# Performance work log

Hardware: AMD Instinct MI355X
Metric: run time of the kernel (lower is better)

## Reference

```python
import jax, jax.numpy as jnp
import numpy as np

B, HW, N, C, F, ITERS = 32, 4096, 16, 128, 512, 3
EPS_LN = 1e-5
EPS_ATTN = 1e-5


def _ln(x, g, b):
    m = x.mean(-1, keepdims=True)
    v = ((x - m) ** 2).mean(-1, keepdims=True)
    return (x - m) / jnp.sqrt(v + EPS_LN) * g + b


def _gru(x, h, wih, whh, bih, bhh):
    # torch.nn.GRUCell math
    gi = x @ wih.T + bih
    gh = h @ whh.T + bhh
    i_r, i_z, i_n = jnp.split(gi, 3, axis=-1)
    h_r, h_z, h_n = jnp.split(gh, 3, axis=-1)
    r = jax.nn.sigmoid(i_r + h_r)
    z = jax.nn.sigmoid(i_z + h_z)
    n = jnp.tanh(i_n + r * h_n)
    return (1.0 - z) * n + z * h


def setup_inputs() -> dict:
    key = jax.random.key(0)
    ks = jax.random.split(key, 16)
    s = 0.02
    d = {
        'inp': jax.random.normal(ks[0], (B, HW, C), jnp.float32),
        'query': jax.random.normal(ks[1], (B, N, C), jnp.float32),
        'ln_kv_g': jnp.ones((C,), jnp.float32),
        'ln_kv_b': jnp.zeros((C,), jnp.float32),
        'Wk': jax.random.normal(ks[2], (C, C), jnp.float32) * s,
        'Wv': jax.random.normal(ks[3], (C, C), jnp.float32) * s,
        'ln_q_g': jnp.ones((C,), jnp.float32),
        'ln_q_b': jnp.zeros((C,), jnp.float32),
        'Wq': jax.random.normal(ks[4], (C, C), jnp.float32) * s,
        'gru_wih': jax.random.normal(ks[5], (3 * C, C), jnp.float32) * s,
        'gru_whh': jax.random.normal(ks[6], (3 * C, C), jnp.float32) * s,
        'gru_bih': jnp.zeros((3 * C,), jnp.float32),
        'gru_bhh': jnp.zeros((3 * C,), jnp.float32),
        'ln2_g': jnp.ones((C,), jnp.float32),
        'ln2_b': jnp.zeros((C,), jnp.float32),
        'ffn_w1': jax.random.normal(ks[7], (F, C), jnp.float32) * s,
        'ffn_b1': jnp.zeros((F,), jnp.float32),
        'ffn_w2': jax.random.normal(ks[8], (C, F), jnp.float32) * s,
        'ffn_b2': jnp.zeros((C,), jnp.float32),
    }
    return d


def reference(inp, query, ln_kv_g, ln_kv_b, Wk, Wv, ln_q_g, ln_q_b, Wq,
              gru_wih, gru_whh, gru_bih, gru_bhh, ln2_g, ln2_b,
              ffn_w1, ffn_b1, ffn_w2, ffn_b2):
    b, n, c = query.shape
    kv = _ln(inp, ln_kv_g, ln_kv_b)
    k = kv @ Wk.T  # (b, hw, c)
    v = kv @ Wv.T  # (b, hw, c)
    scale = c ** -0.5
    q = query
    a0 = None
    for _ in range(ITERS):
        x = q
        qn = _ln(q, ln_q_g, ln_q_b) @ Wq.T
        logit = jnp.einsum('bqc,bkc->bqk', qn * scale, k)  # (b, n, hw)
        a0 = jax.nn.softmax(logit, axis=1)  # inverted: softmax over slots
        a = a0 / (a0.sum(2, keepdims=True) + EPS_ATTN)  # renorm over keys
        u = jnp.einsum('bqk,bkc->bqc', a, v)
        y = _gru(u.reshape(b * n, c), x.reshape(b * n, c),
                 gru_wih, gru_whh, gru_bih, gru_bhh).reshape(b, n, c)
        z = _ln(y, ln2_g, ln2_b)
        ffn = jax.nn.relu(z @ ffn_w1.T + ffn_b1) @ ffn_w2.T + ffn_b2
        q = y + ffn
    return (q, a0)
```

## Files before the change

kernel.cpp:

```cpp
#include <hip/hip_runtime.h>
#include <math.h>

#define B_ 32
#define HW_ 4096
#define N_ 16
#define C_ 128
#define F_ 512
#define ITERS_ 3
#define EPS_LN 1e-5f
#define EPS_ATTN 1e-5f

typedef __attribute__((ext_vector_type(8))) short short8;
typedef __attribute__((ext_vector_type(4))) float f32x4;

static __device__ __forceinline__ unsigned short f2b(float f) {
    union { float f; unsigned u; } v; v.f = f;
    unsigned r = v.u + 0x7fffu + ((v.u >> 16) & 1u);
    return (unsigned short)(r >> 16);
}
static __device__ __forceinline__ float blo(unsigned u) {
    union { unsigned u; float f; } v; v.u = u << 16; return v.f;
}
static __device__ __forceinline__ float bhi(unsigned u) {
    union { unsigned u; float f; } v; v.u = u & 0xffff0000u; return v.f;
}
static __device__ __forceinline__ void gload_lds16(const void* g, void* l) {
    __builtin_amdgcn_global_load_lds(
        (const __attribute__((address_space(1))) unsigned int*)g,
        (__attribute__((address_space(3))) unsigned int*)l, 16, 0, 0);
}

__global__ __launch_bounds__(256) void k_prep(
    const float* __restrict__ Wk, const float* __restrict__ Wv,
    const float* __restrict__ wih, const float* __restrict__ whh,
    const float* __restrict__ w1, const float* __restrict__ w2,
    unsigned short* __restrict__ Wk_sw, unsigned short* __restrict__ Wv_sw,
    unsigned short* __restrict__ wihT, unsigned short* __restrict__ whhT,
    unsigned short* __restrict__ w1T, unsigned short* __restrict__ w2T,
    const float* __restrict__ query, const float* __restrict__ lnqg,
    const float* __restrict__ lnqb, const float* __restrict__ Wq,
    float* __restrict__ wqTf, unsigned short* __restrict__ qn_g)
{
    __shared__ __align__(16) float xq[16 * 128];
    int tid = threadIdx.x;
    int blk = blockIdx.x;
    if (blk < 32) {
        int t = blk * 256 + tid;
        const float* src; unsigned short* dst; int off;
        if (t < 4096) { src = Wk; dst = Wk_sw; off = t; }
        else          { src = Wv; dst = Wv_sw; off = t - 4096; }
        float4 a = ((const float4*)src)[off];
        uint2 p;
        p.x = (unsigned)f2b(a.x) | ((unsigned)f2b(a.y) << 16);
        p.y = (unsigned)f2b(a.z) | ((unsigned)f2b(a.w) << 16);
        int r = off >> 5;
        int j = off & 31;
        int cg = j >> 1, half = j & 1;
        int dsw = r * 128 + (((cg ^ (r & 7)) << 3)) + (half << 2);
        *(uint2*)(dst + dsw) = p;
        return;
    }
    if (blk < 256) {
        const float* src; unsigned short* dst; int o, g, id, Cin;
        if (blk < 80) {
            id = (blk - 32) * 256 + tid;
            g = id / 384; o = id - g * 384;
            src = wih; dst = wihT; Cin = 128;
        } else if (blk < 128) {
            id = (blk - 80) * 256 + tid;
            g = id / 384; o = id - g * 384;
            src = whh; dst = whhT; Cin = 128;
        } else if (blk < 192) {
            id = (blk - 128) * 256 + tid;
            g = id >> 9; o = id & 511;
            src = w1; dst = w1T; Cin = 128;
        } else {
            id = (blk - 192) * 256 + tid;
            g = id >> 7; o = id & 127;
            src = w2; dst = w2T; Cin = 512;
        }
        float4 a = *(const float4*)(src + o * Cin + g * 4);
        uint2 p;
        p.x = (unsigned)f2b(a.x) | ((unsigned)f2b(a.y) << 16);
        p.y = (unsigned)f2b(a.z) | ((unsigned)f2b(a.w) << 16);
        *(uint2*)(dst + id * 4) = p;
        return;
    }
    if (blk >= 288) {
        int t = (blk - 288) * 256 + tid;
        int c = t & 127, g = t >> 7;
        float4 a = *(const float4*)(Wq + c * 128 + g * 4);
        ((float4*)wqTf)[g * 128 + c] = a;
        return;
    }
    int b = blk - 256;
    int n = tid >> 4, part = tid & 15;
    int row = b * 16 + n;
    const float4* x4 = (const float4*)(query + row * 128 + part * 8);
    float4 x0 = x4[0], x1 = x4[1];
    float s = x0.x + x0.y + x0.z + x0.w + x1.x + x1.y + x1.z + x1.w;
    float ss = x0.x * x0.x + x0.y * x0.y + x0.z * x0.z + x0.w * x0.w +
               x1.x * x1.x + x1.y * x1.y + x1.z * x1.z + x1.w * x1.w;
    s += __shfl_xor(s, 1); s += __shfl_xor(s, 2); s += __shfl_xor(s, 4); s += __shfl_xor(s, 8);
    ss += __shfl_xor(ss, 1); ss += __shfl_xor(ss, 2); ss += __shfl_xor(ss, 4); ss += __shfl_xor(ss, 8);
    float mean = s * (1.f / 128.f);
    float var = ss * (1.f / 128.f) - mean * mean;
    float rstd = rsqrtf(var + EPS_LN);
    const float4* g4 = (const float4*)(lnqg + part * 8);
    const float4* b4 = (const float4*)(lnqb + part * 8);
    float4 g0 = g4[0], g1 = g4[1], bb0 = b4[0], bb1 = b4[1];
    float4 o0, o1;
    o0.x = (x0.x - mean) * rstd * g0.x + bb0.x;
    o0.y = (x0.y - mean) * rstd * g0.y + bb0.y;
    o0.z = (x0.z - mean) * rstd * g0.z + bb0.z;
    o0.w = (x0.w - mean) * rstd * g0.w + bb0.w;
    o1.x = (x1.x - mean) * rstd * g1.x + bb1.x;
    o1.y = (x1.y - mean) * rstd * g1.y + bb1.y;
    o1.z = (x1.z - mean) * rstd * g1.z + bb1.z;
    o1.w = (x1.w - mean) * rstd * g1.w + bb1.w;
    float4* xrow = (float4*)&xq[n * 128];
    xrow[part * 2] = o0;
    xrow[part * 2 + 1] = o1;
    __syncthreads();
    float o[8] = {0.f, 0.f, 0.f, 0.f, 0.f, 0.f, 0.f, 0.f};
    const float4* xv4 = (const float4*)&xq[n * 128];
#pragma unroll 4
    for (int j = 0; j < 32; j++) {
        float4 xv = xv4[j];
#pragma unroll
        for (int i = 0; i < 8; i++) {
            float4 w = ((const float4*)(Wq + (part * 8 + i) * 128))[j];
            o[i] += w.x * xv.x + w.y * xv.y + w.z * xv.z + w.w * xv.w;
        }
    }
    const float scale = 0.08838834764831845f;
#pragma unroll
    for (int i = 0; i < 8; i++)
        qn_g[row * 128 + part * 8 + i] = f2b(o[i] * scale);
}

__global__ __launch_bounds__(512, 4) void k_kvproj(
    const float* __restrict__ inp, const float* __restrict__ lng,
    const float* __restrict__ lnb, const unsigned short* __restrict__ Wk_sw,
    const unsigned short* __restrict__ Wv_sw, unsigned short* __restrict__ Kbf,
    unsigned short* __restrict__ Vt)
{
    __shared__ __align__(16) unsigned short W_lds[128 * 128];
    __shared__ __align__(16) unsigned short T_lds[128 * 132];
    const int tid = threadIdx.x;
    const int wave = tid >> 6, lane = tid & 63;
    const int l15 = lane & 15, q4 = lane >> 4;
    const int kof = q4 * 8;
    const int tile0 = blockIdx.x * 128;
    const int b = tile0 >> 12;
    const int hwbase = tile0 & (HW_ - 1);

    {
        const char* gw = (const char*)Wk_sw + wave * 4096 + lane * 16;
        char* lw = (char*)W_lds + wave * 4096;
#pragma unroll
        for (int j = 0; j < 4; j++)
            gload_lds16(gw + j * 1024, lw + j * 1024);
    }

    float x[4][8];
    {
        const float* rowp = inp + (tile0 + (wave << 4) + l15) * C_;
        float s = 0.f, ss = 0.f;
#pragma unroll
        for (int ks = 0; ks < 4; ks++) {
#pragma unroll
            for (int h = 0; h < 2; h++) {
                float4 v = *(const float4*)(rowp + ks * 32 + kof + h * 4);
                x[ks][h * 4 + 0] = v.x; x[ks][h * 4 + 1] = v.y;
                x[ks][h * 4 + 2] = v.z; x[ks][h * 4 + 3] = v.w;
                s += v.x + v.y + v.z + v.w;
                ss += v.x * v.x + v.y * v.y + v.z * v.z + v.w * v.w;
            }
        }
        s += __shfl_xor(s, 16);  s += __shfl_xor(s, 32);
        ss += __shfl_xor(ss, 16); ss += __shfl_xor(ss, 32);
        float mean = s * (1.f / 128.f);
        float var = ss * (1.f / 128.f) - mean * mean;
        float rstd = rsqrtf(var + EPS_LN);
#pragma unroll
        for (int ks = 0; ks < 4; ks++) {
#pragma unroll
            for (int h = 0; h < 2; h++) {
                float4 g = *(const float4*)(lng + ks * 32 + kof + h * 4);
                float4 bb = *(const float4*)(lnb + ks * 32 + kof + h * 4);
                x[ks][h * 4 + 0] = (x[ks][h * 4 + 0] - mean) * rstd * g.x + bb.x;
                x[ks][h * 4 + 1] = (x[ks][h * 4 + 1] - mean) * rstd * g.y + bb.y;
                x[ks][h * 4 + 2] = (x[ks][h * 4 + 2] - mean) * rstd * g.z + bb.z;
                x[ks][h * 4 + 3] = (x[ks][h * 4 + 3] - mean) * rstd * g.w + bb.w;
            }
        }
    }
    short8 af[4];
#pragma unroll
    for (int ks = 0; ks < 4; ks++) {
        union { short8 s8; unsigned u[4]; } p;
#pragma unroll
        for (int j = 0; j < 4; j++)
            p.u[j] = (unsigned)f2b(x[ks][2 * j]) | ((unsigned)f2b(x[ks][2 * j + 1]) << 16);
        af[ks] = p.s8;
    }

    __syncthreads();

    f32x4 acc[8];
#pragma unroll
    for (int nt = 0; nt < 8; nt++) {
        acc[nt] = (f32x4){0.f, 0.f, 0.f, 0.f};
#pragma unroll
        for (int ks = 0; ks < 4; ks++) {
            short8 bf = *(const short8*)&W_lds[(nt * 16 + l15) * 128 + ((ks * 4 + q4) ^ (l15 & 7)) * 8];
            acc[nt] = __builtin_amdgcn_mfma_f32_16x16x32_bf16(af[ks], bf, acc[nt], 0, 0, 0);
        }
    }
#pragma unroll
    for (int nt = 0; nt < 8; nt++) {
        int c = nt * 16 + l15;
#pragma unroll
        for (int i = 0; i < 4; i++)
            T_lds[((wave << 4) + (q4 << 2) + i) * 132 + c] = f2b(acc[nt][i]);
    }
    __syncthreads();

    {
        int row = tid >> 2, part = tid & 3;
        uint4* dst = (uint4*)&Kbf[(b * HW_ + hwbase + row) * C_ + part * 32];
#pragma unroll
        for (int j = 0; j < 4; j++)
            dst[j] = *(const uint4*)&T_lds[row * 132 + part * 32 + j * 8];
    }
    {
        const char* gw = (const char*)Wv_sw + wave * 4096 + lane * 16;
        char* lw = (char*)W_lds + wave * 4096;
#pragma unroll
        for (int j = 0; j < 4; j++)
            gload_lds16(gw + j * 1024, lw + j * 1024);
    }
    __syncthreads();

#pragma unroll
    for (int nt = 0; nt < 8; nt++) {
        acc[nt] = (f32x4){0.f, 0.f, 0.f, 0.f};
#pragma unroll
        for (int ks = 0; ks < 4; ks++) {
            short8 bf = *(const short8*)&W_lds[(nt * 16 + l15) * 128 + ((ks * 4 + q4) ^ (l15 & 7)) * 8];
            acc[nt] = __builtin_amdgcn_mfma_f32_16x16x32_bf16(af[ks], bf, acc[nt], 0, 0, 0);
        }
    }
#pragma unroll
    for (int nt = 0; nt < 8; nt++) {
        int c = nt * 16 + l15;
#pragma unroll
        for (int i = 0; i < 4; i++)
            T_lds[c * 132 + (wave << 4) + (q4 << 2) + i] = f2b(acc[nt][i]);
    }
    __syncthreads();

    {
        int c = tid >> 2, part = tid & 3;
        uint4* dst = (uint4*)&Vt[(b * C_ + c) * HW_ + hwbase + part * 32];
#pragma unroll
        for (int j = 0; j < 4; j++)
            dst[j] = *(const uint4*)&T_lds[c * 132 + part * 32 + j * 8];
    }
}

__global__ __launch_bounds__(256) void k_attn(
    const unsigned short* __restrict__ qn_g, const unsigned short* __restrict__ Kbf,
    const unsigned short* __restrict__ Vt, float* __restrict__ Upart,
    float* __restrict__ rspart, float* __restrict__ a0_out, int last)
{
    __shared__ __align__(16) unsigned short Pb[4][16 * 40];
    __shared__ float rsw[4][16];
    const int b = blockIdx.y, chunk = blockIdx.x;
    const int tid = threadIdx.x;
    const int wave = tid >> 6, lane = tid & 63;
    const int l15 = lane & 15, q4 = lane >> 4;
    const int kof = q4 * 8;
    const int hwb = chunk * 128 + wave * 32;
    const int cbase = wave * 32;

    short8 aq[4];
#pragma unroll
    for (int ks = 0; ks < 4; ks++)
        aq[ks] = *(const short8*)&qn_g[(b * 16 + l15) * 128 + ks * 32 + kof];
    short8 av[2][4];
#pragma unroll
    for (int ct = 0; ct < 2; ct++) {
#pragma unroll
        for (int kc = 0; kc < 4; kc++)
            av[ct][kc] = *(const short8*)&Vt[(b * C_ + cbase + ct * 16 + l15) * HW_
                                             + chunk * 128 + kc * 32 + kof];
    }

    unsigned short* Pw = &Pb[wave][0];
    float rs[4] = {0.f, 0.f, 0.f, 0.f};
#pragma unroll
    for (int s = 0; s < 2; s++) {
        int hwt = hwb + s * 16;
        f32x4 sa = {0.f, 0.f, 0.f, 0.f};
#pragma unroll
        for (int ks = 0; ks < 4; ks++) {
            short8 bk = *(const short8*)&Kbf[(b * HW_ + hwt + l15) * C_ + ks * 32 + kof];
            sa = __builtin_amdgcn_mfma_f32_16x16x32_bf16(aq[ks], bk, sa, 0, 0, 0);
        }
        float mx = fmaxf(fmaxf(sa[0], sa[1]), fmaxf(sa[2], sa[3]));
        mx = fmaxf(mx, __shfl_xor(mx, 16));
        mx = fmaxf(mx, __shfl_xor(mx, 32));
        float e[4]; float ssum = 0.f;
#pragma unroll
        for (int i = 0; i < 4; i++) { e[i] = __expf(sa[i] - mx); ssum += e[i]; }
        ssum += __shfl_xor(ssum, 16);
        ssum += __shfl_xor(ssum, 32);
        float inv = 1.f / ssum;
#pragma unroll
        for (int i = 0; i < 4; i++) {
            float a0v = e[i] * inv;
            rs[i] += a0v;
            if (last) a0_out[(b * 16 + q4 * 4 + i) * HW_ + hwt + l15] = a0v;
            Pw[(q4 * 4 + i) * 40 + s * 16 + l15] = f2b(a0v);
        }
    }
#pragma unroll
    for (int i = 0; i < 4; i++) {
        rs[i] += __shfl_xor(rs[i], 1);
        rs[i] += __shfl_xor(rs[i], 2);
        rs[i] += __shfl_xor(rs[i], 4);
        rs[i] += __shfl_xor(rs[i], 8);
    }
    if (l15 == 0) {
#pragma unroll
        for (int i = 0; i < 4; i++) rsw[wave][q4 * 4 + i] = rs[i];
    }
    __syncthreads();

    f32x4 ua0 = {0.f, 0.f, 0.f, 0.f}, ua1 = {0.f, 0.f, 0.f, 0.f};
#pragma unroll
    for (int kc = 0; kc < 4; kc++) {
        short8 bp = *(const short8*)&Pb[kc][l15 * 40 + kof];
        ua0 = __builtin_amdgcn_mfma_f32_16x16x32_bf16(av[0][kc], bp, ua0, 0, 0, 0);
        ua1 = __builtin_amdgcn_mfma_f32_16x16x32_bf16(av[1][kc], bp, ua1, 0, 0, 0);
    }
    {
        float* up = Upart + (b * 32 + chunk) * 2048;
        *(f32x4*)&up[l15 * 128 + cbase + (q4 << 2)] = ua0;
        *(f32x4*)&up[l15 * 128 + cbase + 16 + (q4 << 2)] = ua1;
        if (tid < 16)
            rspart[(b * 32 + chunk) * 16 + tid] =
                rsw[0][tid] + rsw[1][tid] + rsw[2][tid] + rsw[3][tid];
    }
}

__global__ __launch_bounds__(512) void k_tail(
    const float* __restrict__ Upart, const float* __restrict__ rspart,
    const float* __restrict__ hsrc, float* __restrict__ q_buf,
    const unsigned short* __restrict__ wihT, const unsigned short* __restrict__ whhT,
    const float* __restrict__ bih, const float* __restrict__ bhh,
    const float* __restrict__ ln2g, const float* __restrict__ ln2b,
    const unsigned short* __restrict__ w1T, const float* __restrict__ b1,
    const unsigned short* __restrict__ w2T, const float* __restrict__ b2,
    const float* __restrict__ lnqg, const float* __restrict__ lnqb,
    const float* __restrict__ wqTf, unsigned short* __restrict__ qn_g,
    float* __restrict__ out_q, int last)
{
    __shared__ __align__(16) float red0[512], red1[512];
    __shared__ __align__(16) float u0_l[128], u1_l[128];
    __shared__ __align__(16) float h0_l[128], h1_l[128];
    __shared__ __align__(16) float y0_l[128], y1_l[128];
    __shared__ __align__(16) float z0_l[128], z1_l[128];
    __shared__ __align__(16) float g0_l[768], g1_l[768];
    __shared__ __align__(16) float f0_l[512], f1_l[512];
    __shared__ float srs0, srs1;
    const int tid = threadIdx.x;
    const int row0 = blockIdx.x * 2, row1 = row0 + 1;
    const int b = row0 >> 4, q0 = row0 & 15;

    {
        int c = tid & 127, h = tid >> 7;
        const float* upA = Upart + (b * 32 + h * 8) * 2048 + q0 * 128 + c;
        float a = 0.f, bv = 0.f;
#pragma unroll
        for (int ch = 0; ch < 8; ch++) {
            a  += upA[ch * 2048];
            bv += upA[ch * 2048 + 128];
        }
        red0[tid] = a; red1[tid] = bv;
        if (tid < 128) h0_l[tid] = hsrc[row0 * 128 + tid];
        else if (tid < 256) h1_l[tid - 128] = hsrc[row1 * 128 + (tid - 128)];
        if (tid >= 256 && tid < 288) {
            int t = tid - 256;
            float v = rspart[(b * 32 + t) * 16 + q0];
            v += __shfl_xor(v, 1); v += __shfl_xor(v, 2); v += __shfl_xor(v, 4);
            v += __shfl_xor(v, 8); v += __shfl_xor(v, 16);
            if (t == 0) srs0 = v;
        }
        if (tid >= 320 && tid < 352) {
            int t = tid - 320;
            float v = rspart[(b * 32 + t) * 16 + q0 + 1];
            v += __shfl_xor(v, 1); v += __shfl_xor(v, 2); v += __shfl_xor(v, 4);
            v += __shfl_xor(v, 8); v += __shfl_xor(v, 16);
            if (t == 0) srs1 = v;
        }
    }
    __syncthreads();
    if (tid < 128) {
        float s = red0[tid] + red0[tid + 128] + red0[tid + 256] + red0[tid + 384];
        u0_l[tid] = s / (srs0 + EPS_ATTN);
    } else if (tid < 256) {
        int c = tid - 128;
        float s = red1[c] + red1[c + 128] + red1[c + 256] + red1[c + 384];
        u1_l[c] = s / (srs1 + EPS_ATTN);
    }
    __syncthreads();
    {
        int o = tid;
        const uint2* wp; const float *sA, *sB; float bias;
        if (o < 384) { wp = (const uint2*)wihT + o; sA = u0_l; sB = u1_l; bias = bih[o]; }
        else         { wp = (const uint2*)whhT + (o - 384); sA = h0_l; sB = h1_l; bias = bhh[o - 384]; }
        float fa = 0.f, fb = 0.f;
#pragma unroll 4
        for (int g = 0; g < 32; g++) {
            uint2 w = wp[g * 384];
            float4 a4 = *(const float4*)&sA[g * 4];
            float4 b4 = *(const float4*)&sB[g * 4];
            float w0 = blo(w.x), w1v = bhi(w.x), w2v = blo(w.y), w3 = bhi(w.y);
            fa += w0 * a4.x + w1v * a4.y + w2v * a4.z + w3 * a4.w;
            fb += w0 * b4.x + w1v * b4.y + w2v * b4.z + w3 * b4.w;
        }
        g0_l[o] = fa + bias; g1_l[o] = fb + bias;
        if (tid < 256) {
            int o2 = tid + 512;
            const uint2* wp2 = (const uint2*)whhT + (o2 - 384);
            float fa2 = 0.f, fb2 = 0.f;
#pragma unroll 4
            for (int g = 0; g < 32; g++) {
                uint2 w = wp2[g * 384];
                float4 a4 = *(const float4*)&h0_l[g * 4];
                float4 b4 = *(const float4*)&h1_l[g * 4];
                float w0 = blo(w.x), w1v = bhi(w.x), w2v = blo(w.y), w3 = bhi(w.y);
                fa2 += w0 * a4.x + w1v * a4.y + w2v * a4.z + w3 * a4.w;
                fb2 += w0 * b4.x + w1v * b4.y + w2v * b4.z + w3 * b4.w;
            }
            float bias2 = bhh[o2 - 384];
            g0_l[o2] = fa2 + bias2; g1_l[o2] = fb2 + bias2;
        }
    }
    __syncthreads();
    if (tid < 256) {
        int c = tid & 127, r = tid >> 7;
        const float* gl = r ? g1_l : g0_l;
        const float* hl = r ? h1_l : h0_l;
        float* yl = r ? y1_l : y0_l;
        float ir = gl[c], iz = gl[128 + c], in_ = gl[256 + c];
        float hr = gl[384 + c], hz = gl[512 + c], hn = gl[640 + c];
        float rr = 1.f / (1.f + expf(-(ir + hr)));
        float zz = 1.f / (1.f + expf(-(iz + hz)));
        float nn = tanhf(in_ + rr * hn);
        yl[c] = (1.f - zz) * nn + zz * hl[c];
    }
    __syncthreads();
    {
        int r = tid >> 8;
        const float* yl = r ? y1_l : y0_l;
        int l = tid & 63;
        float v0 = yl[l], v1 = yl[l + 64];
        float s = v0 + v1, ss = v0 * v0 + v1 * v1;
#pragma unroll
        for (int off = 1; off < 64; off <<= 1) {
            s += __shfl_xor(s, off);
            ss += __shfl_xor(ss, off);
        }
        float mean = s * (1.f / 128.f);
        float var = ss * (1.f / 128.f) - mean * mean;
        float rstd = rsqrtf(var + EPS_LN);
        int c = tid & 255;
        if (c < 128) {
            float* zl = r ? z1_l : z0_l;
            zl[c] = (yl[c] - mean) * rstd * ln2g[c] + ln2b[c];
        }
    }
    __syncthreads();
    {
        const uint2* wp = (const uint2*)w1T + tid;
        float fa = 0.f, fb = 0.f;
#pragma unroll 4
        for (int g = 0; g < 32; g++) {
            uint2 w = wp[g * 512];
            float4 za = *(const float4*)&z0_l[g * 4];
            float4 zb = *(const float4*)&z1_l[g * 4];
            float w0 = blo(w.x), w1v = bhi(w.x), w2v = blo(w.y), w3 = bhi(w.y);
            fa += w0 * za.x + w1v * za.y + w2v * za.z + w3 * za.w;
            fb += w0 * zb.x + w1v * zb.y + w2v * zb.z + w3 * zb.w;
        }
        float bb = b1[tid];
        f0_l[tid] = fmaxf(fa + bb, 0.f);
        f1_l[tid] = fmaxf(fb + bb, 0.f);
    }
    __syncthreads();
    {
        int c = tid & 127, k4 = tid >> 7;
        const uint2* wp = (const uint2*)w2T + c;
        float fa = 0.f, fb = 0.f;
#pragma unroll 4
        for (int j = 0; j < 32; j++) {
            int g = k4 * 32 + j;
            uint2 w = wp[g * 128];
            float4 ha = *(const float4*)&f0_l[g * 4];
            float4 hb = *(const float4*)&f1_l[g * 4];
            float w0 = blo(w.x), w1v = bhi(w.x), w2v = blo(w.y), w3 = bhi(w.y);
            fa += w0 * ha.x + w1v * ha.y + w2v * ha.z + w3 * ha.w;
            fb += w0 * hb.x + w1v * hb.y + w2v * hb.z + w3 * hb.w;
        }
        red0[tid] = fa; red1[tid] = fb;
    }
    __syncthreads();
    if (tid < 128) {
        float f2 = red0[tid] + red0[tid + 128] + red0[tid + 256] + red0[tid + 384];
        float qn = y0_l[tid] + f2 + b2[tid];
        u0_l[tid] = qn;
        q_buf[row0 * 128 + tid] = qn;
        if (last) out_q[row0 * 128 + tid] = qn;
    } else if (tid < 256) {
        int c = tid - 128;
        float f2 = red1[c] + red1[c + 128] + red1[c + 256] + red1[c + 384];
        float qn = y1_l[c] + f2 + b2[c];
        u1_l[c] = qn;
        q_buf[row1 * 128 + c] = qn;
        if (last) out_q[row1 * 128 + c] = qn;
    }
    if (last) return;
    __syncthreads();
    {
        int r = tid >> 8;
        const float* yl = r ? u1_l : u0_l;
        int l = tid & 63;
        float v0 = yl[l], v1 = yl[l + 64];
        float s = v0 + v1, ss = v0 * v0 + v1 * v1;
#pragma unroll
        for (int off = 1; off < 64; off <<= 1) {
            s += __shfl_xor(s, off);
            ss += __shfl_xor(ss, off);
        }
        float mean = s * (1.f / 128.f);
        float var = ss * (1.f / 128.f) - mean * mean;
        float rstd = rsqrtf(var + EPS_LN);
        int c = tid & 255;
        if (c < 128) {
            float* zl = r ? z1_l : z0_l;
            zl[c] = (yl[c] - mean) * rstd * lnqg[c] + lnqb[c];
        }
    }
    __syncthreads();
    {
        int c = tid & 127, k4 = tid >> 7;
        const float4* wp = (const float4*)wqTf + c;
        float fa = 0.f, fb = 0.f;
#pragma unroll
        for (int j = 0; j < 8; j++) {
            int g = k4 * 8 + j;
            float4 w = wp[g * 128];
            float4 za = *(const float4*)&z0_l[g * 4];
            float4 zb = *(const float4*)&z1_l[g * 4];
            fa += w.x * za.x + w.y * za.y + w.z * za.z + w.w * za.w;
            fb += w.x * zb.x + w.y * zb.y + w.z * zb.z + w.w * zb.w;
        }
        red0[tid] = fa; red1[tid] = fb;
    }
    __syncthreads();
    if (tid < 128) {
        float qa = red0[tid] + red0[tid + 128] + red0[tid + 256] + red0[tid + 384];
        qn_g[row0 * 128 + tid] = f2b(qa * 0.08838834764831845f);
    } else if (tid < 256) {
        int c = tid - 128;
        float qa = red1[c] + red1[c + 128] + red1[c + 256] + red1[c + 384];
        qn_g[row1 * 128 + c] = f2b(qa * 0.08838834764831845f);
    }
}

extern "C" void kernel_launch(void* const* d_in, const int* in_sizes, int n_in,
                              void* d_out, int out_size, void* d_ws, size_t ws_size,
                              hipStream_t stream) {
    const float* inp     = (const float*)d_in[0];
    const float* query   = (const float*)d_in[1];
    const float* ln_kv_g = (const float*)d_in[2];
    const float* ln_kv_b = (const float*)d_in[3];
    const float* Wk      = (const float*)d_in[4];
    const float* Wv      = (const float*)d_in[5];
    const float* ln_q_g  = (const float*)d_in[6];
    const float* ln_q_b  = (const float*)d_in[7];
    const float* Wq      = (const float*)d_in[8];
    const float* gru_wih = (const float*)d_in[9];
    const float* gru_whh = (const float*)d_in[10];
    const float* gru_bih = (const float*)d_in[11];
    const float* gru_bhh = (const float*)d_in[12];
    const float* ln2_g   = (const float*)d_in[13];
    const float* ln2_b   = (const float*)d_in[14];
    const float* ffn_w1  = (const float*)d_in[15];
    const float* ffn_b1  = (const float*)d_in[16];
    const float* ffn_w2  = (const float*)d_in[17];
    const float* ffn_b2  = (const float*)d_in[18];

    char* ws = (char*)d_ws;
    unsigned short* Kbf    = (unsigned short*)ws;
    unsigned short* Vt     = (unsigned short*)(ws + 33554432);
    float* q_buf           = (float*)(ws + 67108864);
    float* Upart           = (float*)(ws + 67371008);
    float* rspart          = (float*)(ws + 75759616);
    unsigned short* qn_g   = (unsigned short*)(ws + 75825152);
    unsigned short* Wk_sw  = (unsigned short*)(ws + 75956224);
    unsigned short* Wv_sw  = (unsigned short*)(ws + 75988992);
    unsigned short* wihT   = (unsigned short*)(ws + 76021760);
    unsigned short* whhT   = (unsigned short*)(ws + 76120064);
    unsigned short* w1T    = (unsigned short*)(ws + 76218368);
    unsigned short* w2T    = (unsigned short*)(ws + 76349440);
    float* wqTf            = (float*)(ws + 76480512);

    float* out_q  = (float*)d_out;
    float* out_a0 = out_q + B_ * N_ * C_;

    k_prep<<<dim3(304), dim3(256), 0, stream>>>(
        Wk, Wv, gru_wih, gru_whh, ffn_w1, ffn_w2,
        Wk_sw, Wv_sw, wihT, whhT, w1T, w2T,
        query, ln_q_g, ln_q_b, Wq, wqTf, qn_g);
    k_kvproj<<<dim3((B_ * HW_) / 128), dim3(512), 0, stream>>>(
        inp, ln_kv_g, ln_kv_b, Wk_sw, Wv_sw, Kbf, Vt);

    for (int it = 0; it < ITERS_; it++) {
        int last = (it == ITERS_ - 1) ? 1 : 0;
        const float* hsrc = (it == 0) ? query : q_buf;
        k_attn<<<dim3(32, B_), dim3(256), 0, stream>>>(
            qn_g, Kbf, Vt, Upart, rspart, out_a0, last);
        k_tail<<<dim3((B_ * N_) / 2), dim3(512), 0, stream>>>(
            Upart, rspart, hsrc, q_buf, wihT, whhT, gru_bih, gru_bhh,
            ln2_g, ln2_b, w1T, ffn_b1, w2T, ffn_b2,
            ln_q_g, ln_q_b, wqTf, qn_g, out_q, last);
    }
}
```

Measured before the change: 281.2 us.

## Fuse attention and tail iterations into one persistent kernel with per-batch flags

Replaces the six per-iteration k_attn/k_tail launches with a single persistent 256-block kernel. Each group of 8 blocks handles one batch and coordinates through global atomic flags with acquire/release ordering instead of kernel boundaries. This removes launch overhead and lets batches progress independently. In exchange, correctness depends on all 256 blocks being co-resident, there is spin-wait cost, and each block now handles four attention chunks in sequence.

Result: slower. 614.0 us (+118.3%).

```diff
diff --git a/kernel.cpp b/kernel.cpp
--- a/kernel.cpp
+++ b/kernel.cpp
@@ -28,6 +28,19 @@
     __builtin_amdgcn_global_load_lds(
         (const __attribute__((address_space(1))) unsigned int*)g,
         (__attribute__((address_space(3))) unsigned int*)l, 16, 0, 0);
+}
+static __device__ __forceinline__ void postflag(unsigned* f) {
+    __threadfence();
+    __syncthreads();
+    if (threadIdx.x == 0)
+        __hip_atomic_fetch_add(f, 1u, __ATOMIC_RELEASE, __HIP_MEMORY_SCOPE_AGENT);
+}
+static __device__ __forceinline__ void waitflag(unsigned* f, unsigned target) {
+    if (threadIdx.x == 0) {
+        while (__hip_atomic_load(f, __ATOMIC_ACQUIRE, __HIP_MEMORY_SCOPE_AGENT) < target)
+            __builtin_amdgcn_s_sleep(2);
+    }
+    __syncthreads();
 }
 
 __global__ __launch_bounds__(256) void k_prep(
@@ -55,8 +68,8 @@
         p.y = (unsigned)f2b(a.z) | ((unsigned)f2b(a.w) << 16);
         int r = off >> 5;
         int j = off & 31;
-        int cg = j >> 1, half = j & 1;
-        int dsw = r * 128 + (((cg ^ (r & 7)) << 3)) + (half << 2);
+        int cg2 = j >> 1, half = j & 1;
+        int dsw = r * 128 + (((cg2 ^ (r & 7)) << 3)) + (half << 2);
         *(uint2*)(dst + dsw) = p;
         return;
     }
@@ -270,104 +283,22 @@
     }
 }
 
-__global__ __launch_bounds__(256) void k_attn(
-    const unsigned short* __restrict__ qn_g, const unsigned short* __restrict__ Kbf,
-    const unsigned short* __restrict__ Vt, float* __restrict__ Upart,
-    float* __restrict__ rspart, float* __restrict__ a0_out, int last)
-{
-    __shared__ __align__(16) unsigned short Pb[4][16 * 40];
-    __shared__ float rsw[4][16];
-    const int b = blockIdx.y, chunk = blockIdx.x;
-    const int tid = threadIdx.x;
-    const int wave = tid >> 6, lane = tid & 63;
-    const int l15 = lane & 15, q4 = lane >> 4;
-    const int kof = q4 * 8;
-    const int hwb = chunk * 128 + wave * 32;
-    const int cbase = wave * 32;
-
-    short8 aq[4];
-#pragma unroll
-    for (int ks = 0; ks < 4; ks++)
-        aq[ks] = *(const short8*)&qn_g[(b * 16 + l15) * 128 + ks * 32 + kof];
-    short8 av[2][4];
-#pragma unroll
-    for (int ct = 0; ct < 2; ct++) {
-#pragma unroll
-        for (int kc = 0; kc < 4; kc++)
-            av[ct][kc] = *(const short8*)&Vt[(b * C_ + cbase + ct * 16 + l15) * HW_
-                                             + chunk * 128 + kc * 32 + kof];
-    }
-
-    unsigned short* Pw = &Pb[wave][0];
-    float rs[4] = {0.f, 0.f, 0.f, 0.f};
-#pragma unroll
-    for (int s = 0; s < 2; s++) {
-        int hwt = hwb + s * 16;
-        f32x4 sa = {0.f, 0.f, 0.f, 0.f};
-#pragma unroll
-        for (int ks = 0; ks < 4; ks++) {
-            short8 bk = *(const short8*)&Kbf[(b * HW_ + hwt + l15) * C_ + ks * 32 + kof];
-            sa = __builtin_amdgcn_mfma_f32_16x16x32_bf16(aq[ks], bk, sa, 0, 0, 0);
-        }
-        float mx = fmaxf(fmaxf(sa[0], sa[1]), fmaxf(sa[2], sa[3]));
-        mx = fmaxf(mx, __shfl_xor(mx, 16));
-        mx = fmaxf(mx, __shfl_xor(mx, 32));
-        float e[4]; float ssum = 0.f;
-#pragma unroll
-        for (int i = 0; i < 4; i++) { e[i] = __expf(sa[i] - mx); ssum += e[i]; }
-        ssum += __shfl_xor(ssum, 16);
-        ssum += __shfl_xor(ssum, 32);
-        float inv = 1.f / ssum;
-#pragma unroll
-        for (int i = 0; i < 4; i++) {
-            float a0v = e[i] * inv;
-            rs[i] += a0v;
-            if (last) a0_out[(b * 16 + q4 * 4 + i) * HW_ + hwt + l15] = a0v;
-            Pw[(q4 * 4 + i) * 40 + s * 16 + l15] = f2b(a0v);
-        }
-    }
-#pragma unroll
-    for (int i = 0; i < 4; i++) {
-        rs[i] += __shfl_xor(rs[i], 1);
-        rs[i] += __shfl_xor(rs[i], 2);
-        rs[i] += __shfl_xor(rs[i], 4);
-        rs[i] += __shfl_xor(rs[i], 8);
-    }
-    if (l15 == 0) {
-#pragma unroll
-        for (int i = 0; i < 4; i++) rsw[wave][q4 * 4 + i] = rs[i];
-    }
-    __syncthreads();
-
-    f32x4 ua0 = {0.f, 0.f, 0.f, 0.f}, ua1 = {0.f, 0.f, 0.f, 0.f};
-#pragma unroll
-    for (int kc = 0; kc < 4; kc++) {
-        short8 bp = *(const short8*)&Pb[kc][l15 * 40 + kof];
-        ua0 = __builtin_amdgcn_mfma_f32_16x16x32_bf16(av[0][kc], bp, ua0, 0, 0, 0);
-        ua1 = __builtin_amdgcn_mfma_f32_16x16x32_bf16(av[1][kc], bp, ua1, 0, 0, 0);
-    }
-    {
-        float* up = Upart + (b * 32 + chunk) * 2048;
-        *(f32x4*)&up[l15 * 128 + cbase + (q4 << 2)] = ua0;
-        *(f32x4*)&up[l15 * 128 + cbase + 16 + (q4 << 2)] = ua1;
-        if (tid < 16)
-            rspart[(b * 32 + chunk) * 16 + tid] =
-                rsw[0][tid] + rsw[1][tid] + rsw[2][tid] + rsw[3][tid];
-    }
-}
-
-__global__ __launch_bounds__(512) void k_tail(
-    const float* __restrict__ Upart, const float* __restrict__ rspart,
-    const float* __restrict__ hsrc, float* __restrict__ q_buf,
+__global__ __launch_bounds__(512, 2) void k_fused(
+    const float* __restrict__ query, float* __restrict__ q_buf,
+    const unsigned short* __restrict__ Kbf, const unsigned short* __restrict__ Vt,
+    unsigned short* __restrict__ qn_g, float* __restrict__ Upart,
+    float* __restrict__ rspart, float* __restrict__ a0_out,
     const unsigned short* __restrict__ wihT, const unsigned short* __restrict__ whhT,
     const float* __restrict__ bih, const float* __restrict__ bhh,
     const float* __restrict__ ln2g, const float* __restrict__ ln2b,
     const unsigned short* __restrict__ w1T, const float* __restrict__ b1,
     const unsigned short* __restrict__ w2T, const float* __restrict__ b2,
     const float* __restrict__ lnqg, const float* __restrict__ lnqb,
-    const float* __restrict__ wqTf, unsigned short* __restrict__ qn_g,
-    float* __restrict__ out_q, int last)
+    const float* __restrict__ wqTf, float* __restrict__ out_q,
+    unsigned* __restrict__ flags)
 {
+    __shared__ __align__(16) unsigned short Pb[2][4][16 * 40];
+    __shared__ float rsw[2][4][16];
     __shared__ __align__(16) float red0[512], red1[512];
     __shared__ __align__(16) float u0_l[128], u1_l[128];
     __shared__ __align__(16) float h0_l[128], h1_l[128];
@@ -376,209 +307,310 @@
     __shared__ __align__(16) float g0_l[768], g1_l[768];
     __shared__ __align__(16) float f0_l[512], f1_l[512];
     __shared__ float srs0, srs1;
+
     const int tid = threadIdx.x;
-    const int row0 = blockIdx.x * 2, row1 = row0 + 1;
-    const int b = row0 >> 4, q0 = row0 & 15;
-
-    {
-        int c = tid & 127, h = tid >> 7;
-        const float* upA = Upart + (b * 32 + h * 8) * 2048 + q0 * 128 + c;
-        float a = 0.f, bv = 0.f;
-#pragma unroll
-        for (int ch = 0; ch < 8; ch++) {
-            a  += upA[ch * 2048];
-            bv += upA[ch * 2048 + 128];
-        }
-        red0[tid] = a; red1[tid] = bv;
-        if (tid < 128) h0_l[tid] = hsrc[row0 * 128 + tid];
-        else if (tid < 256) h1_l[tid - 128] = hsrc[row1 * 128 + (tid - 128)];
-        if (tid >= 256 && tid < 288) {
-            int t = tid - 256;
-            float v = rspart[(b * 32 + t) * 16 + q0];
-            v += __shfl_xor(v, 1); v += __shfl_xor(v, 2); v += __shfl_xor(v, 4);
-            v += __shfl_xor(v, 8); v += __shfl_xor(v, 16);
-            if (t == 0) srs0 = v;
-        }
-        if (tid >= 320 && tid < 352) {
-            int t = tid - 320;
-            float v = rspart[(b * 32 + t) * 16 + q0 + 1];
-            v += __shfl_xor(v, 1); v += __shfl_xor(v, 2); v += __shfl_xor(v, 4);
-            v += __shfl_xor(v, 8); v += __shfl_xor(v, 16);
-            if (t == 0) srs1 = v;
-        }
-    }
-    __syncthreads();
-    if (tid < 128) {
-        float s = red0[tid] + red0[tid + 128] + red0[tid + 256] + red0[tid + 384];
-        u0_l[tid] = s / (srs0 + EPS_ATTN);
-    } else if (tid < 256) {
-        int c = tid - 128;
-        float s = red1[c] + red1[c + 128] + red1[c + 256] + red1[c + 384];
-        u1_l[c] = s / (srs1 + EPS_ATTN);
-    }
-    __syncthreads();
-    {
-        int o = tid;
-        const uint2* wp; const float *sA, *sB; float bias;
-        if (o < 384) { wp = (const uint2*)wihT + o; sA = u0_l; sB = u1_l; bias = bih[o]; }
-        else         { wp = (const uint2*)whhT + (o - 384); sA = h0_l; sB = h1_l; bias = bhh[o - 384]; }
-        float fa = 0.f, fb = 0.f;
+    const int bid = blockIdx.x;
+    const int b = bid >> 3;
+    unsigned* flagA = flags;
+    unsigned* flagQ = flags + 96;
+
+    const int half = tid >> 8;
+    const int cw = (tid >> 6) & 3;
+    const int lane = tid & 63;
+    const int l15 = lane & 15, q4 = lane >> 4;
+    const int kof = q4 * 8;
+    const int cbase = cw * 32;
+
+    for (int it = 0; it < ITERS_; ++it) {
+        const int last = (it == ITERS_ - 1);
+        if (it > 0) waitflag(&flagQ[it * 32 + b], 8);
+
+        short8 aq[4];
+#pragma unroll
+        for (int ks = 0; ks < 4; ks++)
+            aq[ks] = *(const short8*)&qn_g[(b * 16 + l15) * 128 + ks * 32 + kof];
+        for (int r = 0; r < 2; ++r) {
+            const int chunk = (bid & 7) * 4 + r * 2 + half;
+            const int hwb = chunk * 128 + cw * 32;
+
+            short8 av[2][4];
+#pragma unroll
+            for (int ct = 0; ct < 2; ct++) {
+#pragma unroll
+                for (int kc = 0; kc < 4; kc++)
+                    av[ct][kc] = *(const short8*)&Vt[(b * C_ + cbase + ct * 16 + l15) * HW_
+                                                     + chunk * 128 + kc * 32 + kof];
+            }
+            unsigned short* Pw = &Pb[half][cw][0];
+            float rs[4] = {0.f, 0.f, 0.f, 0.f};
+#pragma unroll
+            for (int s = 0; s < 2; s++) {
+                int hwt = hwb + s * 16;
+                f32x4 sa = {0.f, 0.f, 0.f, 0.f};
+#pragma unroll
+                for (int ks = 0; ks < 4; ks++) {
+                    short8 bk = *(const short8*)&Kbf[(b * HW_ + hwt + l15) * C_ + ks * 32 + kof];
+                    sa = __builtin_amdgcn_mfma_f32_16x16x32_bf16(aq[ks], bk, sa, 0, 0, 0);
+                }
+                float mx = fmaxf(fmaxf(sa[0], sa[1]), fmaxf(sa[2], sa[3]));
+                mx = fmaxf(mx, __shfl_xor(mx, 16));
+                mx = fmaxf(mx, __shfl_xor(mx, 32));
+                float e[4]; float ssum = 0.f;
+#pragma unroll
+                for (int i = 0; i < 4; i++) { e[i] = __expf(sa[i] - mx); ssum += e[i]; }
+                ssum += __shfl_xor(ssum, 16);
+                ssum += __shfl_xor(ssum, 32);
+                float inv = 1.f / ssum;
+#pragma unroll
+                for (int i = 0; i < 4; i++) {
+                    float a0v = e[i] * inv;
+                    rs[i] += a0v;
+                    if (last) a0_out[(b * 16 + q4 * 4 + i) * HW_ + hwt + l15] = a0v;
+                    Pw[(q4 * 4 + i) * 40 + s * 16 + l15] = f2b(a0v);
+                }
+            }
+#pragma unroll
+            for (int i = 0; i < 4; i++) {
+                rs[i] += __shfl_xor(rs[i], 1);
+                rs[i] += __shfl_xor(rs[i], 2);
+                rs[i] += __shfl_xor(rs[i], 4);
+                rs[i] += __shfl_xor(rs[i], 8);
+            }
+            if (l15 == 0) {
+#pragma unroll
+                for (int i = 0; i < 4; i++) rsw[half][cw][q4 * 4 + i] = rs[i];
+            }
+            __syncthreads();
+
+            f32x4 ua0 = {0.f, 0.f, 0.f, 0.f}, ua1 = {0.f, 0.f, 0.f, 0.f};
+#pragma unroll
+            for (int kc = 0; kc < 4; kc++) {
+                short8 bp = *(const short8*)&Pb[half][kc][l15 * 40 + kof];
+                ua0 = __builtin_amdgcn_mfma_f32_16x16x32_bf16(av[0][kc], bp, ua0, 0, 0, 0);
+                ua1 = __builtin_amdgcn_mfma_f32_16x16x32_bf16(av[1][kc], bp, ua1, 0, 0, 0);
+            }
+            {
+                float* up = Upart + (b * 32 + chunk) * 2048;
+                *(f32x4*)&up[l15 * 128 + cbase + (q4 << 2)] = ua0;
+                *(f32x4*)&up[l15 * 128 + cbase + 16 + (q4 << 2)] = ua1;
+                if ((tid & 255) < 16) {
+                    int t = tid & 15;
+                    rspart[(b * 32 + chunk) * 16 + t] =
+                        rsw[half][0][t] + rsw[half][1][t] + rsw[half][2][t] + rsw[half][3][t];
+                }
+            }
+            __syncthreads();
+        }
+        postflag(&flagA[it * 32 + b]);
+        waitflag(&flagA[it * 32 + b], 8);
+
+        {
+            const int row0 = bid * 2, row1 = row0 + 1;
+            const int q0 = row0 & 15;
+            const float* hsrc = (it == 0) ? query : q_buf;
+            {
+                int c = tid & 127, h = tid >> 7;
+                const float* upA = Upart + (b * 32 + h * 8) * 2048 + q0 * 128 + c;
+                float a = 0.f, bv = 0.f;
+#pragma unroll
+                for (int ch = 0; ch < 8; ch++) {
+                    a  += upA[ch * 2048];
+                    bv += upA[ch * 2048 + 128];
+                }
+                red0[tid] = a; red1[tid] = bv;
+                if (tid < 128) h0_l[tid] = hsrc[row0 * 128 + tid];
+                else if (tid < 256) h1_l[tid - 128] = hsrc[row1 * 128 + (tid - 128)];
+                if (tid >= 256 && tid < 288) {
+                    int t = tid - 256;
+                    float v = rspart[(b * 32 + t) * 16 + q0];
+                    v += __shfl_xor(v, 1); v += __shfl_xor(v, 2); v += __shfl_xor(v, 4);
+                    v += __shfl_xor(v, 8); v += __shfl_xor(v, 16);
+                    if (t == 0) srs0 = v;
+                }
+                if (tid >= 320 && tid < 352) {
+                    int t = tid - 320;
+                    float v = rspart[(b * 32 + t) * 16 + q0 + 1];
+                    v += __shfl_xor(v, 1); v += __shfl_xor(v, 2); v += __shfl_xor(v, 4);
+                    v += __shfl_xor(v, 8); v += __shfl_xor(v, 16);
+                    if (t == 0) srs1 = v;
+                }
+            }
+            __syncthreads();
+            if (tid < 128) {
+                float s = red0[tid] + red0[tid + 128] + red0[tid + 256] + red0[tid + 384];
+                u0_l[tid] = s / (srs0 + EPS_ATTN);
+            } else if (tid < 256) {
+                int c = tid - 128;
+                float s = red1[c] + red1[c + 128] + red1[c + 256] + red1[c + 384];
+                u1_l[c] = s / (srs1 + EPS_ATTN);
+            }
+            __syncthreads();
+            {
+                int o = tid;
+                const uint2* wp; const float *sA, *sB; float bias;
+                if (o < 384) { wp = (const uint2*)wihT + o; sA = u0_l; sB = u1_l; bias = bih[o]; }
+                else         { wp = (const uint2*)whhT + (o - 384); sA = h0_l; sB = h1_l; bias = bhh[o - 384]; }
+                float fa = 0.f, fb = 0.f;
 #pragma unroll 4
-        for (int g = 0; g < 32; g++) {
-            uint2 w = wp[g * 384];
-            float4 a4 = *(const float4*)&sA[g * 4];
-            float4 b4 = *(const float4*)&sB[g * 4];
-            float w0 = blo(w.x), w1v = bhi(w.x), w2v = blo(w.y), w3 = bhi(w.y);
-            fa += w0 * a4.x + w1v * a4.y + w2v * a4.z + w3 * a4.w;
-            fb += w0 * b4.x + w1v * b4.y + w2v * b4.z + w3 * b4.w;
-        }
-        g0_l[o] = fa + bias; g1_l[o] = fb + bias;
-        if (tid < 256) {
-            int o2 = tid + 512;
-            const uint2* wp2 = (const uint2*)whhT + (o2 - 384);
-            float fa2 = 0.f, fb2 = 0.f;
+                for (int g = 0; g < 32; g++) {
+                    uint2 w = wp[g * 384];
+                    float4 a4 = *(const float4*)&sA[g * 4];
+                    float4 b4 = *(const float4*)&sB[g * 4];
+                    float w0 = blo(w.x), w1v = bhi(w.x), w2v = blo(w.y), w3 = bhi(w.y);
+                    fa += w0 * a4.x + w1v * a4.y + w2v * a4.z + w3 * a4.w;
+                    fb += w0 * b4.x + w1v * b4.y + w2v * b4.z + w3 * b4.w;
+                }
+                g0_l[o] = fa + bias; g1_l[o] = fb + bias;
+                if (tid < 256) {
+                    int o2 = tid + 512;
+                    const uint2* wp2 = (const uint2*)whhT + (o2 - 384);
+                    float fa2 = 0.f, fb2 = 0.f;
 #pragma unroll 4
-            for (int g = 0; g < 32; g++) {
-                uint2 w = wp2[g * 384];
-                float4 a4 = *(const float4*)&h0_l[g * 4];
-                float4 b4 = *(const float4*)&h1_l[g * 4];
-                float w0 = blo(w.x), w1v = bhi(w.x), w2v = blo(w.y), w3 = bhi(w.y);
-                fa2 += w0 * a4.x + w1v * a4.y + w2v * a4.z + w3 * a4.w;
-                fb2 += w0 * b4.x + w1v * b4.y + w2v * b4.z + w3 * b4.w;
-            }
-            float bias2 = bhh[o2 - 384];
-            g0_l[o2] = fa2 + bias2; g1_l[o2] = fb2 + bias2;
-        }
-    }
-    __syncthreads();
-    if (tid < 256) {
-        int c = tid & 127, r = tid >> 7;
-        const float* gl = r ? g1_l : g0_l;
-        const float* hl = r ? h1_l : h0_l;
-        float* yl = r ? y1_l : y0_l;
-        float ir = gl[c], iz = gl[128 + c], in_ = gl[256 + c];
-        float hr = gl[384 + c], hz = gl[512 + c], hn = gl[640 + c];
-        float rr = 1.f / (1.f + expf(-(ir + hr)));
-        float zz = 1.f / (1.f + expf(-(iz + hz)));
-        float nn = tanhf(in_ + rr * hn);
-        yl[c] = (1.f - zz) * nn + zz * hl[c];
-    }
-    __syncthreads();
-    {
-        int r = tid >> 8;
-        const float* yl = r ? y1_l : y0_l;
-        int l = tid & 63;
-        float v0 = yl[l], v1 = yl[l + 64];
-        float s = v0 + v1, ss = v0 * v0 + v1 * v1;
-#pragma unroll
-        for (int off = 1; off < 64; off <<= 1) {
-            s += __shfl_xor(s, off);
-            ss += __shfl_xor(ss, off);
-        }
-        float mean = s * (1.f / 128.f);
-        float var = ss * (1.f / 128.f) - mean * mean;
-        float rstd = rsqrtf(var + EPS_LN);
-        int c = tid & 255;
-        if (c < 128) {
-            float* zl = r ? z1_l : z0_l;
-            zl[c] = (yl[c] - mean) * rstd * ln2g[c] + ln2b[c];
-        }
-    }
-    __syncthreads();
-    {
-        const uint2* wp = (const uint2*)w1T + tid;
-        float fa = 0.f, fb = 0.f;
+                    for (int g = 0; g < 32; g++) {
+                        uint2 w = wp2[g * 384];
+                        float4 a4 = *(const float4*)&h0_l[g * 4];
+                        float4 b4 = *(const float4*)&h1_l[g * 4];
+                        float w0 = blo(w.x), w1v = bhi(w.x), w2v = blo(w.y), w3 = bhi(w.y);
+                        fa2 += w0 * a4.x + w1v * a4.y + w2v * a4.z + w3 * a4.w;
+                        fb2 += w0 * b4.x + w1v * b4.y + w2v * b4.z + w3 * b4.w;
+                    }
+                    float bias2 = bhh[o2 - 384];
+                    g0_l[o2] = fa2 + bias2; g1_l[o2] = fb2 + bias2;
+                }
+            }
+            __syncthreads();
+            if (tid < 256) {
+                int c = tid & 127, r = tid >> 7;
+                const float* gl = r ? g1_l : g0_l;
+                const float* hl = r ? h1_l : h0_l;
+                float* yl = r ? y1_l : y0_l;
+                float ir = gl[c], iz = gl[128 + c], in_ = gl[256 + c];
+                float hr = gl[384 + c], hz = gl[512 + c], hn = gl[640 + c];
+                float rr = 1.f / (1.f + expf(-(ir + hr)));
+                float zz = 1.f / (1.f + expf(-(iz + hz)));
+                float nn = tanhf(in_ + rr * hn);
+                yl[c] = (1.f - zz) * nn + zz * hl[c];
+            }
+            __syncthreads();
+            {
+                int r = tid >> 8;
+                const float* yl = r ? y1_l : y0_l;
+                int l = tid & 63;
+                float v0 = yl[l], v1 = yl[l + 64];
+                float s = v0 + v1, ss = v0 * v0 + v1 * v1;
+#pragma unroll
+                for (int off = 1; off < 64; off <<= 1) {
+                    s += __shfl_xor(s, off);
+                    ss += __shfl_xor(ss, off);
+                }
+                float mean = s * (1.f / 128.f);
+                float var = ss * (1.f / 128.f) - mean * mean;
+                float rstd = rsqrtf(var + EPS_LN);
+                int c = tid & 255;
+                if (c < 128) {
+                    float* zl = r ? z1_l : z0_l;
+                    zl[c] = (yl[c] - mean) * rstd * ln2g[c] + ln2b[c];
+                }
+            }
+            __syncthreads();
+            {
+                const uint2* wp = (const uint2*)w1T + tid;
+                float fa = 0.f, fb = 0.f;
 #pragma unroll 4
-        for (int g = 0; g < 32; g++) {
-            uint2 w = wp[g * 512];
-            float4 za = *(const float4*)&z0_l[g * 4];
-            float4 zb = *(const float4*)&z1_l[g * 4];
-            float w0 = blo(w.x), w1v = bhi(w.x), w2v = blo(w.y), w3 = bhi(w.y);
-            fa += w0 * za.x + w1v * za.y + w2v * za.z + w3 * za.w;
-            fb += w0 * zb.x + w1v * zb.y + w2v * zb.z + w3 * zb.w;
-        }
-        float bb = b1[tid];
-        f0_l[tid] = fmaxf(fa + bb, 0.f);
-        f1_l[tid] = fmaxf(fb + bb, 0.f);
-    }
-    __syncthreads();
-    {
-        int c = tid & 127, k4 = tid >> 7;
-        const uint2* wp = (const uint2*)w2T + c;
-        float fa = 0.f, fb = 0.f;
+                for (int g = 0; g < 32; g++) {
+                    uint2 w = wp[g * 512];
+                    float4 za = *(const float4*)&z0_l[g * 4];
+                    float4 zb = *(const float4*)&z1_l[g * 4];
+                    float w0 = blo(w.x), w1v = bhi(w.x), w2v = blo(w.y), w3 = bhi(w.y);
+                    fa += w0 * za.x + w1v * za.y + w2v * za.z + w3 * za.w;
+                    fb += w0 * zb.x + w1v * zb.y + w2v * zb.z + w3 * zb.w;
+                }
+                float bb = b1[tid];
+                f0_l[tid] = fmaxf(fa + bb, 0.f);
+                f1_l[tid] = fmaxf(fb + bb, 0.f);
+            }
+            __syncthreads();
+            {
+                int c = tid & 127, k4 = tid >> 7;
+                const uint2* wp = (const uint2*)w2T + c;
+                float fa = 0.f, fb = 0.f;
 #pragma unroll 4
-        for (int j = 0; j < 32; j++) {
-            int g = k4 * 32 + j;
-            uint2 w = wp[g * 128];
-            float4 ha = *(const float4*)&f0_l[g * 4];
-            float4 hb = *(const float4*)&f1_l[g * 4];
-            float w0 = blo(w.x), w1v = bhi(w.x), w2v = blo(w.y), w3 = bhi(w.y);
-            fa += w0 * ha.x + w1v * ha.y + w2v * ha.z + w3 * ha.w;
-            fb += w0 * hb.x + w1v * hb.y + w2v * hb.z + w3 * hb.w;
-        }
-        red0[tid] = fa; red1[tid] = fb;
-    }
-    __syncthreads();
-    if (tid < 128) {
-        float f2 = red0[tid] + red0[tid + 128] + red0[tid + 256] + red0[tid + 384];
-        float qn = y0_l[tid] + f2 + b2[tid];
-        u0_l[tid] = qn;
-        q_buf[row0 * 128 + tid] = qn;
-        if (last) out_q[row0 * 128 + tid] = qn;
-    } else if (tid < 256) {
-        int c = tid - 128;
-        float f2 = red1[c] + red1[c + 128] + red1[c + 256] + red1[c + 384];
-        float qn = y1_l[c] + f2 + b2[c];
-        u1_l[c] = qn;
-        q_buf[row1 * 128 + c] = qn;
-        if (last) out_q[row1 * 128 + c] = qn;
-    }
-    if (last) return;
-    __syncthreads();
-    {
-        int r = tid >> 8;
-        const float* yl = r ? u1_l : u0_l;
-        int l = tid & 63;
-        float v0 = yl[l], v1 = yl[l + 64];
-        float s = v0 + v1, ss = v0 * v0 + v1 * v1;
-#pragma unroll
-        for (int off = 1; off < 64; off <<= 1) {
-            s += __shfl_xor(s, off);
-            ss += __shfl_xor(ss, off);
-        }
-        float mean = s * (1.f / 128.f);
-        float var = ss * (1.f / 128.f) - mean * mean;
-        float rstd = rsqrtf(var + EPS_LN);
-        int c = tid & 255;
-        if (c < 128) {
-            float* zl = r ? z1_l : z0_l;
-            zl[c] = (yl[c] - mean) * rstd * lnqg[c] + lnqb[c];
-        }
-    }
-    __syncthreads();
-    {
-        int c = tid & 127, k4 = tid >> 7;
-        const float4* wp = (const float4*)wqTf + c;
-        float fa = 0.f, fb = 0.f;
-#pragma unroll
-        for (int j = 0; j < 8; j++) {
-            int g = k4 * 8 + j;
-            float4 w = wp[g * 128];
-            float4 za = *(const float4*)&z0_l[g * 4];
-            float4 zb = *(const float4*)&z1_l[g * 4];
-            fa += w.x * za.x + w.y * za.y + w.z * za.z + w.w * za.w;
-            fb += w.x * zb.x + w.y * zb.y + w.z * zb.z + w.w * zb.w;
-        }
-        red0[tid] = fa; red1[tid] = fb;
-    }
-    __syncthreads();
-    if (tid < 128) {
-        float qa = red0[tid] + red0[tid + 128] + red0[tid + 256] + red0[tid + 384];
-        qn_g[row0 * 128 + tid] = f2b(qa * 0.08838834764831845f);
-    } else if (tid < 256) {
-        int c = tid - 128;
-        float qa = red1[c] + red1[c + 128] + red1[c + 256] + red1[c + 384];
-        qn_g[row1 * 128 + c] = f2b(qa * 0.08838834764831845f);
+                for (int j = 0; j < 32; j++) {
+                    int g = k4 * 32 + j;
+                    uint2 w = wp[g * 128];
+                    float4 ha = *(const float4*)&f0_l[g * 4];
+                    float4 hb = *(const float4*)&f1_l[g * 4];
+                    float w0 = blo(w.x), w1v = bhi(w.x), w2v = blo(w.y), w3 = bhi(w.y);
+                    fa += w0 * ha.x + w1v * ha.y + w2v * ha.z + w3 * ha.w;
+                    fb += w0 * hb.x + w1v * hb.y + w2v * hb.z + w3 * hb.w;
+                }
+                red0[tid] = fa; red1[tid] = fb;
+            }
+            __syncthreads();
+            if (tid < 128) {
+                float f2 = red0[tid] + red0[tid + 128] + red0[tid + 256] + red0[tid + 384];
+                float qn = y0_l[tid] + f2 + b2[tid];
+                u0_l[tid] = qn;
+                q_buf[row0 * 128 + tid] = qn;
+                if (last) out_q[row0 * 128 + tid] = qn;
+            } else if (tid < 256) {
+                int c = tid - 128;
+                float f2 = red1[c] + red1[c + 128] + red1[c + 256] + red1[c + 384];
+                float qn = y1_l[c] + f2 + b2[c];
+                u1_l[c] = qn;
+                q_buf[row1 * 128 + c] = qn;
+                if (last) out_q[row1 * 128 + c] = qn;
+            }
+            if (!last) {
+                __syncthreads();
+                {
+                    int r = tid >> 8;
+                    const float* yl = r ? u1_l : u0_l;
+                    int l = tid & 63;
+                    float v0 = yl[l], v1 = yl[l + 64];
+                    float s = v0 + v1, ss = v0 * v0 + v1 * v1;
+#pragma unroll
+                    for (int off = 1; off < 64; off <<= 1) {
+                        s += __shfl_xor(s, off);
+                        ss += __shfl_xor(ss, off);
+                    }
+                    float mean = s * (1.f / 128.f);
+                    float var = ss * (1.f / 128.f) - mean * mean;
+                    float rstd = rsqrtf(var + EPS_LN);
+                    int c = tid & 255;
+                    if (c < 128) {
+                        float* zl = r ? z1_l : z0_l;
+                        zl[c] = (yl[c] - mean) * rstd * lnqg[c] + lnqb[c];
+                    }
+                }
+                __syncthreads();
+                {
+                    int c = tid & 127, k4 = tid >> 7;
+                    const float4* wp = (const float4*)wqTf + c;
+                    float fa = 0.f, fb = 0.f;
+#pragma unroll
+                    for (int j = 0; j < 8; j++) {
+                        int g = k4 * 8 + j;
+                        float4 w = wp[g * 128];
+                        float4 za = *(const float4*)&z0_l[g * 4];
+                        float4 zb = *(const float4*)&z1_l[g * 4];
+                        fa += w.x * za.x + w.y * za.y + w.z * za.z + w.w * za.w;
+                        fb += w.x * zb.x + w.y * zb.y + w.z * zb.z + w.w * zb.w;
+                    }
+                    red0[tid] = fa; red1[tid] = fb;
+                }
+                __syncthreads();
+                if (tid < 128) {
+                    float qa = red0[tid] + red0[tid + 128] + red0[tid + 256] + red0[tid + 384];
+                    qn_g[row0 * 128 + tid] = f2b(qa * 0.08838834764831845f);
+                } else if (tid < 256) {
+                    int c = tid - 128;
+                    float qa = red1[c] + red1[c + 128] + red1[c + 256] + red1[c + 384];
+                    qn_g[row1 * 128 + c] = f2b(qa * 0.08838834764831845f);
+                }
+                postflag(&flagQ[(it + 1) * 32 + b]);
+            }
+        }
     }
 }
 
@@ -619,25 +651,21 @@
     unsigned short* w1T    = (unsigned short*)(ws + 76218368);
     unsigned short* w2T    = (unsigned short*)(ws + 76349440);
     float* wqTf            = (float*)(ws + 76480512);
+    unsigned* flags        = (unsigned*)(ws + 76546048);
 
     float* out_q  = (float*)d_out;
     float* out_a0 = out_q + B_ * N_ * C_;
 
+    hipMemsetAsync(flags, 0, 768, stream);
     k_prep<<<dim3(304), dim3(256), 0, stream>>>(
         Wk, Wv, gru_wih, gru_whh, ffn_w1, ffn_w2,
         Wk_sw, Wv_sw, wihT, whhT, w1T, w2T,
         query, ln_q_g, ln_q_b, Wq, wqTf, qn_g);
     k_kvproj<<<dim3((B_ * HW_) / 128), dim3(512), 0, stream>>>(
         inp, ln_kv_g, ln_kv_b, Wk_sw, Wv_sw, Kbf, Vt);
-
-    for (int it = 0; it < ITERS_; it++) {
-        int last = (it == ITERS_ - 1) ? 1 : 0;
-        const float* hsrc = (it == 0) ? query : q_buf;
-        k_attn<<<dim3(32, B_), dim3(256), 0, stream>>>(
-            qn_g, Kbf, Vt, Upart, rspart, out_a0, last);
-        k_tail<<<dim3((B_ * N_) / 2), dim3(512), 0, stream>>>(
-            Upart, rspart, hsrc, q_buf, wihT, whhT, gru_bih, gru_bhh,
-            ln2_g, ln2_b, w1T, ffn_b1, w2T, ffn_b2,
-            ln_q_g, ln_q_b, wqTf, qn_g, out_q, last);
-    }
-}
+    k_fused<<<dim3(256), dim3(512), 0, stream>>>(
+        query, q_buf, Kbf, Vt, qn_g, Upart, rspart, out_a0,
+        wihT, whhT, gru_bih, gru_bhh, ln2_g, ln2_b,
+        w1T, ffn_b1, w2T, ffn_b2, ln_q_g, ln_q_b,
+        wqTf, out_q, flags);
+}
```
